# Kernel optimization log

Measured on AMD Instinct MI355X. Metric: run time of the kernel, lower is better.

The kernel has to match this reference:

```python
import jax, jax.numpy as jnp
import numpy as np

EPS = 1e-5


def gcn_conv(x, edge_index, W, b):
    # PyG GCNConv: h = x @ W; add self-loops; symmetric deg^-1/2 normalization; scatter-add to dst; + bias
    n = x.shape[0]
    h = x @ W  # [N, out]
    loops = jnp.arange(n, dtype=edge_index.dtype)
    src = jnp.concatenate([edge_index[0], loops])
    dst = jnp.concatenate([edge_index[1], loops])
    deg = jax.ops.segment_sum(jnp.ones(src.shape[0], dtype=h.dtype), dst, num_segments=n)
    dinv = jnp.where(deg > 0, jax.lax.rsqrt(jnp.maximum(deg, 1e-12)), 0.0)
    norm = dinv[src] * dinv[dst]  # [E+N]
    out = jax.ops.segment_sum(h[src] * norm[:, None], dst, num_segments=n)
    return out + b


def setup_inputs() -> dict:
    key = jax.random.key(0)
    ks = jax.random.split(key, 10)
    N, E = 50000, 800000
    IN, HID, OUT = 128, 128, 64
    x = jax.random.normal(ks[0], (N, IN), dtype=jnp.float32)
    edge_index1 = jax.random.randint(ks[1], (2, E), 0, N, dtype=jnp.int64)
    edge_index2 = jax.random.randint(ks[2], (2, E), 0, N, dtype=jnp.int64)
    s1 = 1.0 / np.sqrt(IN)
    s2 = 1.0 / np.sqrt(HID)
    W1 = jax.random.uniform(ks[3], (IN, HID), jnp.float32, -s1, s1)
    b1 = jax.random.uniform(ks[4], (HID,), jnp.float32, -s1, s1)
    gamma = jnp.ones((HID,), jnp.float32)
    beta = jnp.zeros((HID,), jnp.float32)
    W2 = jax.random.uniform(ks[5], (HID, OUT), jnp.float32, -s2, s2)
    b2 = jax.random.uniform(ks[6], (OUT,), jnp.float32, -s2, s2)
    return {"x": x, "edge_index1": edge_index1, "edge_index2": edge_index2,
            "W1": W1, "b1": b1, "gamma": gamma, "beta": beta, "W2": W2, "b2": b2}


def reference(x, edge_index1, edge_index2, W1, b1, gamma, beta, W2, b2):
    # layer 1: GCNConv -> (save hidden) -> BatchNorm1d (batch stats) -> ReLU -> dropout (identity, deterministic)
    h = gcn_conv(x, edge_index1, W1, b1)
    hidden = h
    mean = jnp.mean(h, axis=0)
    var = jnp.mean((h - mean) ** 2, axis=0)  # biased var, as torch BN uses for normalization
    h = (h - mean) * jax.lax.rsqrt(var + EPS) * gamma + beta
    h = jax.nn.relu(h)
    # layer 2: GCNConv (no norm/act on last layer)
    out = gcn_conv(h, edge_index2, W2, b2)
    return (out, hidden)
```

## Files before the change

kernel.cpp:

```cpp
#include <hip/hip_runtime.h>

#define GN 50000
#define GE 800000
#define HID 128
#define OUTC 64
#define NBK 196
#define NW  196
#define EPW 4096
#define PCAP 5888
#define A1B 2048

#define OFF_H1    0
#define OFF_H2    3200000
#define OFF_DINV1 4800000
#define OFF_DINV2 4850000
#define OFF_ROW1  4900000
#define OFF_ROW2  4950004
#define OFF_HIST  5000008
#define OFF_TOT   5076840
#define OFF_BBASE 5077232
#define OFF_BN    5077632
#define OFF_PART  5078144
#define OFF_SRC1  5606528
#define OFF_SRC2  6406528

typedef __attribute__((ext_vector_type(8))) short bf16x8;
typedef __attribute__((ext_vector_type(4))) float f32x4;

__device__ inline unsigned bf16rne(float f) {
  unsigned u = __float_as_uint(f);
  return (u + 0x7FFFu + ((u >> 16) & 1u)) >> 16;
}
__device__ inline unsigned pack2(float a, float b) {
  return bf16rne(a) | (bf16rne(b) << 16);
}
__device__ inline float bflo(unsigned w) { return __uint_as_float(w << 16); }
__device__ inline float bfhi(unsigned w) { return __uint_as_float(w & 0xFFFF0000u); }
__device__ inline float bfs(unsigned short w) { return __uint_as_float(((unsigned)w) << 16); }

__global__ __launch_bounds__(256) void p1hist_kernel(const int* __restrict__ e1,
    const int* __restrict__ e2, int* __restrict__ hist) {
  __shared__ int h[NBK];
  int g = blockIdx.y, w = blockIdx.x;
  const int* dst = (g ? e2 : e1) + GE;
  for (int i = threadIdx.x; i < NBK; i += 256) h[i] = 0;
  __syncthreads();
  int i0 = w * EPW, iend = i0 + EPW; if (iend > GE) iend = GE;
  for (int i = i0 + threadIdx.x * 4; i < iend; i += 1024) {
    int4 d4 = *(const int4*)&dst[i];
    atomicAdd(&h[d4.x >> 8], 1);
    atomicAdd(&h[d4.y >> 8], 1);
    atomicAdd(&h[d4.z >> 8], 1);
    atomicAdd(&h[d4.w >> 8], 1);
  }
  __syncthreads();
  int* out = hist + ((size_t)g * NW + w) * NBK;
  for (int i = threadIdx.x; i < NBK; i += 256) out[i] = h[i];
}

__global__ __launch_bounds__(256) void histscanA_kernel(int* __restrict__ hist,
    int* __restrict__ tot) {
  __shared__ int lds[256];
  int b = blockIdx.x, g = blockIdx.y, t = threadIdx.x;
  int* col = hist + (size_t)g * NW * NBK + b;
  int v = (t < NW) ? col[(size_t)t * NBK] : 0;
  lds[t] = v;
  __syncthreads();
  for (int off = 1; off < 256; off <<= 1) {
    int u = (t >= off) ? lds[t - off] : 0;
    __syncthreads();
    lds[t] += u;
    __syncthreads();
  }
  if (t < NW) col[(size_t)t * NBK] = lds[t] - v;
  if (t == NW - 1) tot[g * NBK + b] = lds[t];
}

__global__ __launch_bounds__(256) void histscanB_kernel(const int* __restrict__ tot,
    int* __restrict__ bbase) {
  __shared__ int lds[256];
  int t = threadIdx.x;
  for (int g = 0; g < 2; ++g) {
    int v = (t < NBK) ? tot[g * NBK + t] : 0;
    int orig = v;
    lds[t] = v;
    __syncthreads();
    for (int off = 1; off < 256; off <<= 1) {
      int u = (t >= off) ? lds[t - off] : 0;
      __syncthreads();
      lds[t] += u;
      __syncthreads();
    }
    if (t < NBK) bbase[g * (NBK + 1) + t] = lds[t] - orig;
    if (t == NBK - 1) bbase[g * (NBK + 1) + NBK] = lds[t];
    __syncthreads();
  }
}

__global__ __launch_bounds__(256) void p1scat_kernel(const int* __restrict__ e1,
    const int* __restrict__ e2, const int* __restrict__ hist,
    const int* __restrict__ bbase, int* __restrict__ pb1, int* __restrict__ pb2) {
  __shared__ int off[NBK];
  int g = blockIdx.y, w = blockIdx.x;
  const int* e = g ? e2 : e1;
  int* pb = g ? pb2 : pb1;
  const int* hrow = hist + ((size_t)g * NW + w) * NBK;
  const int* bb = bbase + g * (NBK + 1);
  for (int i = threadIdx.x; i < NBK; i += 256) off[i] = bb[i] + hrow[i];
  __syncthreads();
  int i0 = w * EPW, iend = i0 + EPW; if (iend > GE) iend = GE;
  for (int i = i0 + threadIdx.x * 4; i < iend; i += 1024) {
    int4 s4 = *(const int4*)&e[i];
    int4 d4 = *(const int4*)&e[GE + i];
    int p0 = atomicAdd(&off[d4.x >> 8], 1);
    pb[p0] = s4.x | ((d4.x & 255) << 16);
    int p1 = atomicAdd(&off[d4.y >> 8], 1);
    pb[p1] = s4.y | ((d4.y & 255) << 16);
    int p2 = atomicAdd(&off[d4.z >> 8], 1);
    pb[p2] = s4.z | ((d4.z & 255) << 16);
    int p3 = atomicAdd(&off[d4.w >> 8], 1);
    pb[p3] = s4.w | ((d4.w & 255) << 16);
  }
}

__global__ __launch_bounds__(256) void p2sort_kernel(const int* __restrict__ pb1,
    const int* __restrict__ pb2, const int* __restrict__ bbase,
    int* __restrict__ row1, int* __restrict__ row2,
    float* __restrict__ dinv1, float* __restrict__ dinv2,
    int* __restrict__ src1, int* __restrict__ src2) {
  __shared__ int stage[PCAP];
  __shared__ int lcnt[256], lc2[256], arr[256];
  __shared__ int lrow[257];
  int g = blockIdx.y, b = blockIdx.x, t = threadIdx.x;
  const int* pb = g ? pb2 : pb1;
  const int* bb = bbase + g * (NBK + 1);
  int* row = g ? row2 : row1;
  float* dinv = g ? dinv2 : dinv1;
  int* src = g ? src2 : src1;
  int lo = b << 8, hi = lo + 256; if (hi > GN) hi = GN;
  int nn = hi - lo;
  int base = bb[b], end = bb[b + 1], L = end - base;
  lcnt[t] = 0; lc2[t] = 0;
  __syncthreads();
  for (int i = base + t; i < end; i += 256)
    atomicAdd(&lcnt[((unsigned)pb[i]) >> 16], 1);
  __syncthreads();
  int v = lcnt[t];
  arr[t] = v;
  __syncthreads();
  for (int off = 1; off < 256; off <<= 1) {
    int u = (t >= off) ? arr[t - off] : 0;
    __syncthreads();
    arr[t] += u;
    __syncthreads();
  }
  lrow[t] = arr[t] - v;
  if (t == 255) lrow[256] = arr[255];
  __syncthreads();
  if (t < nn) {
    row[lo + t] = base + lrow[t];
    dinv[lo + t] = rsqrtf(1.0f + (float)lcnt[t]);
  }
  if (b == NBK - 1 && t == 0) row[GN] = end;
  if (L <= PCAP) {
    for (int i = base + t; i < end; i += 256) {
      unsigned p = (unsigned)pb[i];
      int ld = p >> 16;
      int rk = atomicAdd(&lc2[ld], 1);
      stage[lrow[ld] + rk] = (int)(p & 0xFFFFu);
    }
    __syncthreads();
    for (int i = t; i < L; i += 256) src[base + i] = stage[i];
  } else {
    for (int i = base + t; i < end; i += 256) {
      unsigned p = (unsigned)pb[i];
      int ld = p >> 16;
      int rk = atomicAdd(&lc2[ld], 1);
      src[base + lrow[ld] + rk] = (int)(p & 0xFFFFu);
    }
  }
}

__global__ __launch_bounds__(256) void gemm1_kernel(const float* __restrict__ A,
    const float* __restrict__ W1, const float* __restrict__ dinv1,
    unsigned short* __restrict__ h1u) {
  __shared__ unsigned a_lds[64 * 68];
  __shared__ unsigned w_lds[128 * 68];
  int t = threadIdx.x;
  int row0 = blockIdx.x * 64;
  for (int i = t; i < 128 * 64; i += 256) {
    int k2 = i >> 7, n = i & 127;
    w_lds[n * 68 + k2] = pack2(W1[(2 * k2) * 128 + n], W1[(2 * k2 + 1) * 128 + n]);
  }
  for (int i = t; i < 64 * 32; i += 256) {
    int m = i >> 5, k4 = i & 31;
    int gr = row0 + m;
    float4 v = (gr < GN) ? ((const float4*)A)[(size_t)gr * 32 + k4]
                         : make_float4(0.f, 0.f, 0.f, 0.f);
    unsigned* dst = &a_lds[m * 68 + k4 * 2];
    dst[0] = pack2(v.x, v.y);
    dst[1] = pack2(v.z, v.w);
  }
  __syncthreads();
  int lane = t & 63, w = t >> 6;
  int n16 = lane & 15, quad = lane >> 4;
  int mbase = (w & 1) * 32;
  int nbase = (w >> 1) * 64;
  f32x4 acc[2][4] = {};
  const unsigned short* als = (const unsigned short*)a_lds;
  const unsigned short* wls = (const unsigned short*)w_lds;
  #pragma unroll
  for (int ks = 0; ks < 4; ++ks) {
    int k0 = ks * 32 + quad * 8;
    bf16x8 a0 = *(const bf16x8*)(als + (mbase + n16) * 136 + k0);
    bf16x8 a1 = *(const bf16x8*)(als + (mbase + 16 + n16) * 136 + k0);
    #pragma unroll
    for (int nt = 0; nt < 4; ++nt) {
      bf16x8 bf = *(const bf16x8*)(wls + (nbase + nt * 16 + n16) * 136 + k0);
      acc[0][nt] = __builtin_amdgcn_mfma_f32_16x16x32_bf16(a0, bf, acc[0][nt], 0, 0, 0);
      acc[1][nt] = __builtin_amdgcn_mfma_f32_16x16x32_bf16(a1, bf, acc[1][nt], 0, 0, 0);
    }
  }
  #pragma unroll
  for (int mt = 0; mt < 2; ++mt) {
    #pragma unroll
    for (int r = 0; r < 4; ++r) {
      int row_g = row0 + mbase + mt * 16 + quad * 4 + r;
      if (row_g < GN) {
        float dv = dinv1[row_g];
        #pragma unroll
        for (int nt = 0; nt < 4; ++nt) {
          int col = nbase + nt * 16 + n16;
          h1u[(size_t)row_g * 128 + col] = (unsigned short)bf16rne(dv * acc[mt][nt][r]);
        }
      }
    }
  }
}

__global__ __launch_bounds__(256) void gemm2_kernel(const float* __restrict__ A,
    const float* __restrict__ W2, const float* __restrict__ scale,
    const float* __restrict__ shift, const float* __restrict__ dinv2,
    unsigned short* __restrict__ h2u) {
  __shared__ unsigned a_lds[64 * 68];
  __shared__ unsigned w_lds[64 * 68];
  __shared__ float sc[128], sh[128];
  int t = threadIdx.x;
  if (t < 128) { sc[t] = scale[t]; sh[t] = shift[t]; }
  int row0 = blockIdx.x * 64;
  for (int i = t; i < 64 * 64; i += 256) {
    int k2 = i >> 6, n = i & 63;
    w_lds[n * 68 + k2] = pack2(W2[(2 * k2) * 64 + n], W2[(2 * k2 + 1) * 64 + n]);
  }
  __syncthreads();
  for (int i = t; i < 64 * 32; i += 256) {
    int m = i >> 5, k4 = i & 31;
    int gr = row0 + m;
    float4 v = (gr < GN) ? ((const float4*)A)[(size_t)gr * 32 + k4]
                         : make_float4(0.f, 0.f, 0.f, 0.f);
    int c = k4 * 4;
    v.x = fmaxf(fmaf(v.x, sc[c],     sh[c]),     0.f);
    v.y = fmaxf(fmaf(v.y, sc[c + 1], sh[c + 1]), 0.f);
    v.z = fmaxf(fmaf(v.z, sc[c + 2], sh[c + 2]), 0.f);
    v.w = fmaxf(fmaf(v.w, sc[c + 3], sh[c + 3]), 0.f);
    unsigned* dst = &a_lds[m * 68 + k4 * 2];
    dst[0] = pack2(v.x, v.y);
    dst[1] = pack2(v.z, v.w);
  }
  __syncthreads();
  int lane = t & 63, w = t >> 6;
  int n16 = lane & 15, quad = lane >> 4;
  f32x4 acc[4] = {};
  const unsigned short* als = (const unsigned short*)a_lds;
  const unsigned short* wls = (const unsigned short*)w_lds;
  #pragma unroll
  for (int ks = 0; ks < 4; ++ks) {
    int k0 = ks * 32 + quad * 8;
    bf16x8 af = *(const bf16x8*)(als + (w * 16 + n16) * 136 + k0);
    #pragma unroll
    for (int nt = 0; nt < 4; ++nt) {
      bf16x8 bf = *(const bf16x8*)(wls + (nt * 16 + n16) * 136 + k0);
      acc[nt] = __builtin_amdgcn_mfma_f32_16x16x32_bf16(af, bf, acc[nt], 0, 0, 0);
    }
  }
  #pragma unroll
  for (int r = 0; r < 4; ++r) {
    int row_g = row0 + w * 16 + quad * 4 + r;
    if (row_g < GN) {
      float dv = dinv2[row_g];
      #pragma unroll
      for (int nt = 0; nt < 4; ++nt) {
        int col = nt * 16 + n16;
        h2u[(size_t)row_g * 64 + col] = (unsigned short)bf16rne(dv * acc[nt][r]);
      }
    }
  }
}

__global__ __launch_bounds__(256) void agg1_kernel(const unsigned* __restrict__ h1b,
    const int* __restrict__ row, const int* __restrict__ srcs,
    const float* __restrict__ dinv, const float* __restrict__ b1,
    float* __restrict__ hidden, float* __restrict__ part) {
  __shared__ float ps[256];
  int t = threadIdx.x;
  int lane = t & 63;
  float2 b = ((const float2*)b1)[lane];
  float sx = 0.f, sy = 0.f, qx = 0.f, qy = 0.f;
  int wid = (blockIdx.x * 256 + t) >> 6;
  for (int d = wid; d < GN; d += A1B * 4) {
    float di = dinv[d];
    unsigned sw = h1b[(size_t)d * 64 + lane];
    float ax = bflo(sw), ay = bfhi(sw);
    int e0 = row[d], e1 = row[d + 1];
    int i = e0;
    while ((i & 3) && i < e1) {
      unsigned v = h1b[(size_t)srcs[i] * 64 + lane];
      ax += bflo(v); ay += bfhi(v);
      ++i;
    }
    for (; i + 8 <= e1; i += 8) {
      int4 sa = *(const int4*)&srcs[i];
      int4 sb = *(const int4*)&srcs[i + 4];
      unsigned v0 = h1b[(size_t)sa.x * 64 + lane], v1 = h1b[(size_t)sa.y * 64 + lane];
      unsigned v2 = h1b[(size_t)sa.z * 64 + lane], v3 = h1b[(size_t)sa.w * 64 + lane];
      unsigned v4 = h1b[(size_t)sb.x * 64 + lane], v5 = h1b[(size_t)sb.y * 64 + lane];
      unsigned v6 = h1b[(size_t)sb.z * 64 + lane], v7 = h1b[(size_t)sb.w * 64 + lane];
      ax += bflo(v0); ay += bfhi(v0);
      ax += bflo(v1); ay += bfhi(v1);
      ax += bflo(v2); ay += bfhi(v2);
      ax += bflo(v3); ay += bfhi(v3);
      ax += bflo(v4); ay += bfhi(v4);
      ax += bflo(v5); ay += bfhi(v5);
      ax += bflo(v6); ay += bfhi(v6);
      ax += bflo(v7); ay += bfhi(v7);
    }
    if (i + 4 <= e1) {
      int4 sa = *(const int4*)&srcs[i];
      unsigned v0 = h1b[(size_t)sa.x * 64 + lane], v1 = h1b[(size_t)sa.y * 64 + lane];
      unsigned v2 = h1b[(size_t)sa.z * 64 + lane], v3 = h1b[(size_t)sa.w * 64 + lane];
      ax += bflo(v0); ay += bfhi(v0);
      ax += bflo(v1); ay += bfhi(v1);
      ax += bflo(v2); ay += bfhi(v2);
      ax += bflo(v3); ay += bfhi(v3);
      i += 4;
    }
    for (; i < e1; ++i) {
      unsigned v = h1b[(size_t)srcs[i] * 64 + lane];
      ax += bflo(v); ay += bfhi(v);
    }
    float ox = ax * di + b.x, oy = ay * di + b.y;
    float2 o; o.x = ox; o.y = oy;
    ((float2*)(hidden + (size_t)d * 128))[lane] = o;
    sx += ox; sy += oy; qx += ox * ox; qy += oy * oy;
  }
  float* pout = part + (size_t)blockIdx.x * 256;
  ps[t] = sx; __syncthreads();
  if (t < 64) pout[2 * t] = ps[t] + ps[t + 64] + ps[t + 128] + ps[t + 192];
  __syncthreads();
  ps[t] = sy; __syncthreads();
  if (t < 64) pout[2 * t + 1] = ps[t] + ps[t + 64] + ps[t + 128] + ps[t + 192];
  __syncthreads();
  ps[t] = qx; __syncthreads();
  if (t < 64) pout[128 + 2 * t] = ps[t] + ps[t + 64] + ps[t + 128] + ps[t + 192];
  __syncthreads();
  ps[t] = qy; __syncthreads();
  if (t < 64) pout[128 + 2 * t + 1] = ps[t] + ps[t + 64] + ps[t + 128] + ps[t + 192];
}

__global__ __launch_bounds__(256) void bn_reduceA_kernel(const float* __restrict__ part,
    float* __restrict__ partA) {
  int r = blockIdx.x, t = threadIdx.x;
  float s = 0.f;
  for (int k = 0; k < A1B / 64; ++k)
    s += part[((size_t)r * (A1B / 64) + k) * 256 + t];
  partA[r * 256 + t] = s;
}

__global__ __launch_bounds__(128) void bn_final_kernel(const float* __restrict__ partA,
    const float* __restrict__ gamma, const float* __restrict__ beta,
    float* __restrict__ scale, float* __restrict__ shift) {
  int c = threadIdx.x;
  float S = 0.f, Q = 0.f;
  for (int r = 0; r < 64; ++r) {
    S += partA[r * 256 + c];
    Q += partA[r * 256 + 128 + c];
  }
  float mean = S * (1.0f / GN);
  float var = Q * (1.0f / GN) - mean * mean;
  float istd = rsqrtf(var + 1e-5f);
  float g = gamma[c] * istd;
  scale[c] = g;
  shift[c] = beta[c] - mean * g;
}

__global__ __launch_bounds__(256) void agg2_kernel(const unsigned short* __restrict__ h2b,
    const int* __restrict__ row, const int* __restrict__ srcs,
    const float* __restrict__ dinv, const float* __restrict__ b2,
    float* __restrict__ out) {
  int wave = (blockIdx.x * 256 + threadIdx.x) >> 6;
  int lane = threadIdx.x & 63;
  if (wave >= GN) return;
  int d = wave;
  float di = dinv[d];
  float acc = bfs(h2b[(size_t)d * 64 + lane]);
  int e0 = row[d], e1 = row[d + 1];
  int i = e0;
  while ((i & 3) && i < e1) {
    acc += bfs(h2b[(size_t)srcs[i] * 64 + lane]);
    ++i;
  }
  for (; i + 8 <= e1; i += 8) {
    int4 sa = *(const int4*)&srcs[i];
    int4 sb = *(const int4*)&srcs[i + 4];
    float v0 = bfs(h2b[(size_t)sa.x * 64 + lane]), v1 = bfs(h2b[(size_t)sa.y * 64 + lane]);
    float v2 = bfs(h2b[(size_t)sa.z * 64 + lane]), v3 = bfs(h2b[(size_t)sa.w * 64 + lane]);
    float v4 = bfs(h2b[(size_t)sb.x * 64 + lane]), v5 = bfs(h2b[(size_t)sb.y * 64 + lane]);
    float v6 = bfs(h2b[(size_t)sb.z * 64 + lane]), v7 = bfs(h2b[(size_t)sb.w * 64 + lane]);
    acc += v0 + v1 + v2 + v3 + v4 + v5 + v6 + v7;
  }
  if (i + 4 <= e1) {
    int4 sa = *(const int4*)&srcs[i];
    acc += bfs(h2b[(size_t)sa.x * 64 + lane]) + bfs(h2b[(size_t)sa.y * 64 + lane])
         + bfs(h2b[(size_t)sa.z * 64 + lane]) + bfs(h2b[(size_t)sa.w * 64 + lane]);
    i += 4;
  }
  for (; i < e1; ++i)
    acc += bfs(h2b[(size_t)srcs[i] * 64 + lane]);
  out[(size_t)d * 64 + lane] = acc * di + b2[lane];
}

extern "C" void kernel_launch(void* const* d_in, const int* in_sizes, int n_in,
                              void* d_out, int out_size, void* d_ws, size_t ws_size,
                              hipStream_t stream) {
  const float* x     = (const float*)d_in[0];
  const int*   e1    = (const int*)d_in[1];
  const int*   e2    = (const int*)d_in[2];
  const float* W1    = (const float*)d_in[3];
  const float* b1    = (const float*)d_in[4];
  const float* gamma = (const float*)d_in[5];
  const float* beta  = (const float*)d_in[6];
  const float* W2    = (const float*)d_in[7];
  const float* b2    = (const float*)d_in[8];

  float* out    = (float*)d_out;
  float* hidden = out + (size_t)GN * OUTC;

  float*          ws    = (float*)d_ws;
  unsigned*       h1b   = (unsigned*)(ws + OFF_H1);
  unsigned*       h2b   = (unsigned*)(ws + OFF_H2);
  float*          dinv1 = ws + OFF_DINV1;
  float*          dinv2 = ws + OFF_DINV2;
  int*            row1  = (int*)(ws + OFF_ROW1);
  int*            row2  = (int*)(ws + OFF_ROW2);
  int*            hist  = (int*)(ws + OFF_HIST);
  int*            tot   = (int*)(ws + OFF_TOT);
  int*            bbase = (int*)(ws + OFF_BBASE);
  float*          bnbuf = ws + OFF_BN;
  float*          part  = ws + OFF_PART;
  float*          partA = ws + OFF_HIST;
  int*            src1  = (int*)(ws + OFF_SRC1);
  int*            src2  = (int*)(ws + OFF_SRC2);
  int*            pb1   = (int*)h2b;
  int*            pb2   = pb1 + GE;

  p1hist_kernel<<<dim3(NW, 2), 256, 0, stream>>>(e1, e2, hist);
  histscanA_kernel<<<dim3(NBK, 2), 256, 0, stream>>>(hist, tot);
  histscanB_kernel<<<1, 256, 0, stream>>>(tot, bbase);
  p1scat_kernel<<<dim3(NW, 2), 256, 0, stream>>>(e1, e2, hist, bbase, pb1, pb2);
  p2sort_kernel<<<dim3(NBK, 2), 256, 0, stream>>>(pb1, pb2, bbase,
                                                  row1, row2, dinv1, dinv2, src1, src2);

  gemm1_kernel<<<(GN + 63) / 64, 256, 0, stream>>>(x, W1, dinv1,
                                                   (unsigned short*)h1b);
  agg1_kernel<<<A1B, 256, 0, stream>>>(h1b, row1, src1, dinv1, b1, hidden, part);

  bn_reduceA_kernel<<<64, 256, 0, stream>>>(part, partA);
  bn_final_kernel<<<1, 128, 0, stream>>>(partA, gamma, beta, bnbuf, bnbuf + 128);

  gemm2_kernel<<<(GN + 63) / 64, 256, 0, stream>>>(hidden, W2, bnbuf, bnbuf + 128,
                                                   dinv2, (unsigned short*)h2b);
  agg2_kernel<<<(GN * 64 + 255) / 256, 256, 0, stream>>>(
      (const unsigned short*)h2b, row2, src2, dinv2, b2, out);
}
```

Baseline: 227.8 us.

## Replace two-pass bucket sort CSR build with global atomic counting sort

Replaces the bucketed two-pass radix-style CSR construction (per-workgroup LDS histograms, partition buffer, per-bucket LDS sort) with a direct global-atomic degree histogram, a three-stage scan over node counts, and a scatter that uses global atomics on per-node write offsets. This removes the intermediate partition buffer and the second sort pass, cutting memory traffic and one heavy kernel. In exchange it relies on contended global atomics and random scattered writes, and the order of sources within a row becomes nondeterministic, which can change float summation order.

```diff
diff --git a/kernel.cpp b/kernel.cpp
--- a/kernel.cpp
+++ b/kernel.cpp
@@ -4,25 +4,25 @@
 #define GE 800000
 #define HID 128
 #define OUTC 64
-#define NBK 196
 #define NW  196
 #define EPW 4096
-#define PCAP 5888
+#define NSB 196
 #define A1B 2048
 
 #define OFF_H1    0
 #define OFF_H2    3200000
+#define OFF_CNT   3200000
+#define OFF_WOFF  3300000
+#define OFF_BSUM  3400000
 #define OFF_DINV1 4800000
 #define OFF_DINV2 4850000
 #define OFF_ROW1  4900000
 #define OFF_ROW2  4950004
-#define OFF_HIST  5000008
-#define OFF_TOT   5076840
-#define OFF_BBASE 5077232
 #define OFF_BN    5077632
 #define OFF_PART  5078144
-#define OFF_SRC1  5606528
-#define OFF_SRC2  6406528
+#define OFF_PARTA 5602432
+#define OFF_SRC1  5618816
+#define OFF_SRC2  6418816
 
 typedef __attribute__((ext_vector_type(8))) short bf16x8;
 typedef __attribute__((ext_vector_type(4))) float f32x4;
@@ -38,32 +38,33 @@
 __device__ inline float bfhi(unsigned w) { return __uint_as_float(w & 0xFFFF0000u); }
 __device__ inline float bfs(unsigned short w) { return __uint_as_float(((unsigned)w) << 16); }
 
-__global__ __launch_bounds__(256) void p1hist_kernel(const int* __restrict__ e1,
-    const int* __restrict__ e2, int* __restrict__ hist) {
-  __shared__ int h[NBK];
+__global__ __launch_bounds__(256) void zero_kernel(int* __restrict__ cnt) {
+  int i = blockIdx.x * 256 + threadIdx.x;
+  if (i < 2 * GN) cnt[i] = 0;
+}
+
+__global__ __launch_bounds__(256) void ghist_kernel(const int* __restrict__ e1,
+    const int* __restrict__ e2, int* __restrict__ cnt) {
   int g = blockIdx.y, w = blockIdx.x;
   const int* dst = (g ? e2 : e1) + GE;
-  for (int i = threadIdx.x; i < NBK; i += 256) h[i] = 0;
-  __syncthreads();
+  int* c = cnt + g * GN;
   int i0 = w * EPW, iend = i0 + EPW; if (iend > GE) iend = GE;
   for (int i = i0 + threadIdx.x * 4; i < iend; i += 1024) {
     int4 d4 = *(const int4*)&dst[i];
-    atomicAdd(&h[d4.x >> 8], 1);
-    atomicAdd(&h[d4.y >> 8], 1);
-    atomicAdd(&h[d4.z >> 8], 1);
-    atomicAdd(&h[d4.w >> 8], 1);
-  }
-  __syncthreads();
-  int* out = hist + ((size_t)g * NW + w) * NBK;
-  for (int i = threadIdx.x; i < NBK; i += 256) out[i] = h[i];
-}
-
-__global__ __launch_bounds__(256) void histscanA_kernel(int* __restrict__ hist,
-    int* __restrict__ tot) {
+    atomicAdd(&c[d4.x], 1);
+    atomicAdd(&c[d4.y], 1);
+    atomicAdd(&c[d4.z], 1);
+    atomicAdd(&c[d4.w], 1);
+  }
+}
+
+__global__ __launch_bounds__(256) void scanA_kernel(const int* __restrict__ cnt,
+    int* __restrict__ row1, int* __restrict__ row2,
+    float* __restrict__ dinv1, float* __restrict__ dinv2, int* __restrict__ bsum) {
   __shared__ int lds[256];
-  int b = blockIdx.x, g = blockIdx.y, t = threadIdx.x;
-  int* col = hist + (size_t)g * NW * NBK + b;
-  int v = (t < NW) ? col[(size_t)t * NBK] : 0;
+  int g = blockIdx.y, b = blockIdx.x, t = threadIdx.x;
+  int d = b * 256 + t;
+  int v = (d < GN) ? cnt[g * GN + d] : 0;
   lds[t] = v;
   __syncthreads();
   for (int off = 1; off < 256; off <<= 1) {
@@ -72,16 +73,20 @@
     lds[t] += u;
     __syncthreads();
   }
-  if (t < NW) col[(size_t)t * NBK] = lds[t] - v;
-  if (t == NW - 1) tot[g * NBK + b] = lds[t];
-}
-
-__global__ __launch_bounds__(256) void histscanB_kernel(const int* __restrict__ tot,
-    int* __restrict__ bbase) {
+  int* row = g ? row2 : row1;
+  float* dinv = g ? dinv2 : dinv1;
+  if (d < GN) {
+    row[d] = lds[t] - v;
+    dinv[d] = rsqrtf(1.0f + (float)v);
+  }
+  if (t == 255) bsum[g * NSB + b] = lds[t];
+}
+
+__global__ __launch_bounds__(256) void scanB_kernel(int* __restrict__ bsum) {
   __shared__ int lds[256];
   int t = threadIdx.x;
   for (int g = 0; g < 2; ++g) {
-    int v = (t < NBK) ? tot[g * NBK + t] : 0;
+    int v = (t < NSB) ? bsum[g * NSB + t] : 0;
     int orig = v;
     lds[t] = v;
     __syncthreads();
@@ -91,93 +96,39 @@
       lds[t] += u;
       __syncthreads();
     }
-    if (t < NBK) bbase[g * (NBK + 1) + t] = lds[t] - orig;
-    if (t == NBK - 1) bbase[g * (NBK + 1) + NBK] = lds[t];
+    if (t < NSB) bsum[g * NSB + t] = lds[t] - orig;
     __syncthreads();
   }
 }
 
-__global__ __launch_bounds__(256) void p1scat_kernel(const int* __restrict__ e1,
-    const int* __restrict__ e2, const int* __restrict__ hist,
-    const int* __restrict__ bbase, int* __restrict__ pb1, int* __restrict__ pb2) {
-  __shared__ int off[NBK];
+__global__ __launch_bounds__(256) void scanC_kernel(const int* __restrict__ bsum,
+    int* __restrict__ row1, int* __restrict__ row2, int* __restrict__ woff) {
+  int g = blockIdx.y, b = blockIdx.x, t = threadIdx.x;
+  int d = b * 256 + t;
+  int* row = g ? row2 : row1;
+  if (d < GN) {
+    int r = row[d] + bsum[g * NSB + b];
+    row[d] = r;
+    woff[g * GN + d] = r;
+  }
+  if (g == 0 && b == 0 && t == 0) { row1[GN] = GE; row2[GN] = GE; }
+}
+
+__global__ __launch_bounds__(256) void scat_kernel(const int* __restrict__ e1,
+    const int* __restrict__ e2, int* __restrict__ woff,
+    int* __restrict__ src1, int* __restrict__ src2) {
   int g = blockIdx.y, w = blockIdx.x;
   const int* e = g ? e2 : e1;
-  int* pb = g ? pb2 : pb1;
-  const int* hrow = hist + ((size_t)g * NW + w) * NBK;
-  const int* bb = bbase + g * (NBK + 1);
-  for (int i = threadIdx.x; i < NBK; i += 256) off[i] = bb[i] + hrow[i];
-  __syncthreads();
+  int* wo = woff + g * GN;
+  int* src = g ? src2 : src1;
   int i0 = w * EPW, iend = i0 + EPW; if (iend > GE) iend = GE;
   for (int i = i0 + threadIdx.x * 4; i < iend; i += 1024) {
     int4 s4 = *(const int4*)&e[i];
     int4 d4 = *(const int4*)&e[GE + i];
-    int p0 = atomicAdd(&off[d4.x >> 8], 1);
-    pb[p0] = s4.x | ((d4.x & 255) << 16);
-    int p1 = atomicAdd(&off[d4.y >> 8], 1);
-    pb[p1] = s4.y | ((d4.y & 255) << 16);
-    int p2 = atomicAdd(&off[d4.z >> 8], 1);
-    pb[p2] = s4.z | ((d4.z & 255) << 16);
-    int p3 = atomicAdd(&off[d4.w >> 8], 1);
-    pb[p3] = s4.w | ((d4.w & 255) << 16);
-  }
-}
-
-__global__ __launch_bounds__(256) void p2sort_kernel(const int* __restrict__ pb1,
-    const int* __restrict__ pb2, const int* __restrict__ bbase,
-    int* __restrict__ row1, int* __restrict__ row2,
-    float* __restrict__ dinv1, float* __restrict__ dinv2,
-    int* __restrict__ src1, int* __restrict__ src2) {
-  __shared__ int stage[PCAP];
-  __shared__ int lcnt[256], lc2[256], arr[256];
-  __shared__ int lrow[257];
-  int g = blockIdx.y, b = blockIdx.x, t = threadIdx.x;
-  const int* pb = g ? pb2 : pb1;
-  const int* bb = bbase + g * (NBK + 1);
-  int* row = g ? row2 : row1;
-  float* dinv = g ? dinv2 : dinv1;
-  int* src = g ? src2 : src1;
-  int lo = b << 8, hi = lo + 256; if (hi > GN) hi = GN;
-  int nn = hi - lo;
-  int base = bb[b], end = bb[b + 1], L = end - base;
-  lcnt[t] = 0; lc2[t] = 0;
-  __syncthreads();
-  for (int i = base + t; i < end; i += 256)
-    atomicAdd(&lcnt[((unsigned)pb[i]) >> 16], 1);
-  __syncthreads();
-  int v = lcnt[t];
-  arr[t] = v;
-  __syncthreads();
-  for (int off = 1; off < 256; off <<= 1) {
-    int u = (t >= off) ? arr[t - off] : 0;
-    __syncthreads();
-    arr[t] += u;
-    __syncthreads();
-  }
-  lrow[t] = arr[t] - v;
-  if (t == 255) lrow[256] = arr[255];
-  __syncthreads();
-  if (t < nn) {
-    row[lo + t] = base + lrow[t];
-    dinv[lo + t] = rsqrtf(1.0f + (float)lcnt[t]);
-  }
-  if (b == NBK - 1 && t == 0) row[GN] = end;
-  if (L <= PCAP) {
-    for (int i = base + t; i < end; i += 256) {
-      unsigned p = (unsigned)pb[i];
-      int ld = p >> 16;
-      int rk = atomicAdd(&lc2[ld], 1);
-      stage[lrow[ld] + rk] = (int)(p & 0xFFFFu);
-    }
-    __syncthreads();
-    for (int i = t; i < L; i += 256) src[base + i] = stage[i];
-  } else {
-    for (int i = base + t; i < end; i += 256) {
-      unsigned p = (unsigned)pb[i];
-      int ld = p >> 16;
-      int rk = atomicAdd(&lc2[ld], 1);
-      src[base + lrow[ld] + rk] = (int)(p & 0xFFFFu);
-    }
+    src[atomicAdd(&wo[d4.x], 1)] = s4.x;
+    src[atomicAdd(&wo[d4.y], 1)] = s4.y;
+    src[atomicAdd(&wo[d4.z], 1)] = s4.z;
+    src[atomicAdd(&wo[d4.w], 1)] = s4.w;
   }
 }
 
@@ -448,27 +399,25 @@
   float*          ws    = (float*)d_ws;
   unsigned*       h1b   = (unsigned*)(ws + OFF_H1);
   unsigned*       h2b   = (unsigned*)(ws + OFF_H2);
+  int*            cnt   = (int*)(ws + OFF_CNT);
+  int*            woff  = (int*)(ws + OFF_WOFF);
+  int*            bsum  = (int*)(ws + OFF_BSUM);
   float*          dinv1 = ws + OFF_DINV1;
   float*          dinv2 = ws + OFF_DINV2;
   int*            row1  = (int*)(ws + OFF_ROW1);
   int*            row2  = (int*)(ws + OFF_ROW2);
-  int*            hist  = (int*)(ws + OFF_HIST);
-  int*            tot   = (int*)(ws + OFF_TOT);
-  int*            bbase = (int*)(ws + OFF_BBASE);
   float*          bnbuf = ws + OFF_BN;
   float*          part  = ws + OFF_PART;
-  float*          partA = ws + OFF_HIST;
+  float*          partA = ws + OFF_PARTA;
   int*            src1  = (int*)(ws + OFF_SRC1);
   int*            src2  = (int*)(ws + OFF_SRC2);
-  int*            pb1   = (int*)h2b;
-  int*            pb2   = pb1 + GE;
-
-  p1hist_kernel<<<dim3(NW, 2), 256, 0, stream>>>(e1, e2, hist);
-  histscanA_kernel<<<dim3(NBK, 2), 256, 0, stream>>>(hist, tot);
-  histscanB_kernel<<<1, 256, 0, stream>>>(tot, bbase);
-  p1scat_kernel<<<dim3(NW, 2), 256, 0, stream>>>(e1, e2, hist, bbase, pb1, pb2);
-  p2sort_kernel<<<dim3(NBK, 2), 256, 0, stream>>>(pb1, pb2, bbase,
-                                                  row1, row2, dinv1, dinv2, src1, src2);
+
+  zero_kernel<<<(2 * GN + 255) / 256, 256, 0, stream>>>(cnt);
+  ghist_kernel<<<dim3(NW, 2), 256, 0, stream>>>(e1, e2, cnt);
+  scanA_kernel<<<dim3(NSB, 2), 256, 0, stream>>>(cnt, row1, row2, dinv1, dinv2, bsum);
+  scanB_kernel<<<1, 256, 0, stream>>>(bsum);
+  scanC_kernel<<<dim3(NSB, 2), 256, 0, stream>>>(bsum, row1, row2, woff);
+  scat_kernel<<<dim3(NW, 2), 256, 0, stream>>>(e1, e2, woff, src1, src2);
 
   gemm1_kernel<<<(GN + 63) / 64, 256, 0, stream>>>(x, W1, dinv1,
                                                    (unsigned short*)h1b);
```

After: 370.1 us. +62.5%, slower.
